# Performance work log

Hardware: AMD Instinct MI355X
Metric: run time of the kernel (lower is better)

## Reference

```python
import jax, jax.numpy as jnp
import numpy as np

NUM_LEVELS = 8
CODEBOOK_SIZE = 1024
EMBED_DIM = 256
BETA = 0.25
N_TOKENS = 65536
EPS = 1e-6


def setup_inputs() -> dict:
    key = jax.random.key(0)
    kz, kc = jax.random.split(key)
    z = jax.random.normal(kz, (N_TOKENS, EMBED_DIM), dtype=jnp.float32)
    # per-level init std = 1 / 2**i, matching nn.init.normal_ in __init__
    scales = (0.5 ** jnp.arange(NUM_LEVELS, dtype=jnp.float32))[:, None, None]
    codebooks = jax.random.normal(kc, (NUM_LEVELS, CODEBOOK_SIZE, EMBED_DIM), dtype=jnp.float32) * scales
    return {"z": z, "codebooks": codebooks}


def _normalize(v):
    # F.normalize(p=2, dim=-1, eps=1e-6): v / max(||v||, eps)
    return v / jnp.maximum(jnp.linalg.norm(v, axis=-1, keepdims=True), EPS)


def _rotation_trick(x, quantized):
    sg = jax.lax.stop_gradient
    u = _normalize(x)
    q = _normalize(quantized)
    w = _normalize(u + q)
    xw_dot = jnp.sum(x * sg(w), axis=-1, keepdims=True)
    xu_dot = jnp.sum(x * sg(u), axis=-1, keepdims=True)
    return x - 2.0 * xw_dot * sg(w) + 2.0 * xu_dot * sg(q)


def reference(z, codebooks):
    sg = jax.lax.stop_gradient
    residual = z
    quantized_sum = jnp.zeros_like(z)
    indices_list = []
    total_codebook_loss = jnp.float32(0.0)
    total_commitment_loss = jnp.float32(0.0)
    for lvl in range(NUM_LEVELS):
        c = codebooks[lvl]  # [K, D]
        # squared-euclidean distances up to constant ||x||^2 (argmin-equivalent, as in source)
        c_sq = jnp.sum(c * c, axis=1)                      # [K]
        dists = c_sq - 2.0 * (residual @ c.T)              # [N, K]
        min_idx = jnp.argmin(dists, axis=-1)               # [N]
        indices_list.append(min_idx)
        z_q_local = c[min_idx]                             # gather [N, D]
        total_codebook_loss = total_codebook_loss + jnp.mean((z_q_local - sg(residual)) ** 2)
        total_commitment_loss = total_commitment_loss + jnp.mean((sg(z_q_local) - residual) ** 2)
        # training path uses the rotation-trick estimator
        z_q_st = _rotation_trick(residual, z_q_local)
        residual = residual - z_q_st
        quantized_sum = quantized_sum + z_q_local
    indices = jnp.stack(indices_list, axis=-1)             # [N, L]
    loss = total_codebook_loss + BETA * total_commitment_loss
    # perplexity (codebook utilization entropy)
    flat = indices.reshape(-1)
    counts = jnp.zeros((CODEBOOK_SIZE,), jnp.float32).at[flat].add(1.0)
    probs = counts / jnp.float32(flat.size)
    safe = jnp.where(probs > 0, probs, 1.0)
    entropy = -jnp.sum(probs * jnp.log(safe))
    perplexity = jnp.exp(entropy)
    # straight-through output
    z_q = z + sg(quantized_sum - z)
    return (z_q, indices, loss, total_codebook_loss, total_commitment_loss, perplexity)
```

## Files before the change

kernel.cpp:

```cpp
#include <hip/hip_runtime.h>

#define N_TOK 65536
#define DIM 256
#define KCB 1024
#define NLVL 8
#define TPB 32
#define ND_OUT (N_TOK * DIM)
#define IDX_OFF ND_OUT
#define SC_OFF (ND_OUT + N_TOK * NLVL)
#define EPSV 1e-6f

typedef _Float16 half8 __attribute__((ext_vector_type(8)));
typedef float f32x4 __attribute__((ext_vector_type(4)));

__device__ __forceinline__ float wave_red(float v) {
    v += __shfl_xor(v, 32, 64);
    v += __shfl_xor(v, 16, 64);
    v += __shfl_xor(v, 8, 64);
    v += __shfl_xor(v, 4, 64);
    v += __shfl_xor(v, 2, 64);
    v += __shfl_xor(v, 1, 64);
    return v;
}

__device__ __forceinline__ unsigned int ordf(float d) {
    unsigned int u = __float_as_uint(d);
    return (u & 0x80000000u) ? ~u : (u ^ 0x80000000u);
}

__global__ __launch_bounds__(256) void k_prep(const float* __restrict__ cbs,
                                              half8* __restrict__ ws_b) {
    const int lvl = blockIdx.x >> 6, ntg = blockIdx.x & 63;
    const int lane = threadIdx.x & 63, sg = threadIdx.x >> 6;
    const float sc = (float)(1 << (lvl + 5));
#pragma unroll
    for (int ss = 0; ss < 2; ++ss) {
        const int s = sg + ss * 4;
        const int code = ntg * 16 + (lane & 15);
        const int d0 = s * 32 + (lane >> 4) * 8;
        const float* p = cbs + ((size_t)(lvl * KCB + code)) * DIM + d0;
        const float4 va = *(const float4*)p;
        const float4 vb = *(const float4*)(p + 4);
        float f[8] = {va.x, va.y, va.z, va.w, vb.x, vb.y, vb.z, vb.w};
        half8 h, l;
#pragma unroll
        for (int j = 0; j < 8; ++j) {
            float fs = f[j] * sc;
            _Float16 hh = (_Float16)fs;
            h[j] = hh;
            l[j] = (_Float16)(fs - (float)hh);
        }
        const size_t base = ((size_t)((lvl * 8 + s) * 64 + ntg)) * 128;
        ws_b[base + lane] = h;
        ws_b[base + 64 + lane] = l;
    }
}

__global__ __launch_bounds__(256) void k_csq(const float* __restrict__ cbs,
                                             float* __restrict__ csq_s,
                                             int* __restrict__ gcounts,
                                             float* __restrict__ gloss) {
    const int tid = threadIdx.x;
    const int wv = tid >> 6, lane = tid & 63;
    const int code = blockIdx.x * 4 + wv;
    const float4 v = *(const float4*)(cbs + (size_t)code * DIM + lane * 4);
    float s = v.x * v.x + v.y * v.y + v.z * v.z + v.w * v.w;
    s = wave_red(s);
    const int lvl = code >> 10;
    if (lane == 0) csq_s[code] = s * (float)(1 << (10 + lvl));
    if (blockIdx.x == 0) {
#pragma unroll
        for (int i = 0; i < 4; ++i) gcounts[tid + i * 256] = 0;
        if (tid == 0) *gloss = 0.f;
    }
}

__global__ __launch_bounds__(512, 4) void k_main(const float* __restrict__ z,
                                                 const float* __restrict__ cbs,
                                                 const half8* __restrict__ ws_b,
                                                 const float* __restrict__ csq_s,
                                                 float* __restrict__ out,
                                                 int* __restrict__ gcounts,
                                                 float* __restrict__ gloss) {
    __shared__ __align__(16) float Rld[TPB * DIM];
    __shared__ __align__(16) half8 Afrag[2048];
    __shared__ unsigned long long keyBuf[8][TPB + 1];
    __shared__ int idxBuf[TPB * NLVL];
    __shared__ int hist[KCB];
    __shared__ float wpart[8];

    const int tid = threadIdx.x;
    const int lane = tid & 63, w = tid >> 6;
    const int l15 = lane & 15, qd = lane >> 4;
    const int t0 = blockIdx.x * TPB;

#pragma unroll
    for (int i = 0; i < 4; ++i) {
        int fi = tid + i * 512;
        int t = fi >> 6, k4 = fi & 63;
        float4 v = *(const float4*)(z + (size_t)(t0 + t) * DIM + k4 * 4);
        v.x *= 32.f; v.y *= 32.f; v.z *= 32.f; v.w *= 32.f;
        *(float4*)&Rld[t * DIM + ((k4 ^ (t & 15)) << 2)] = v;
    }
#pragma unroll
    for (int i = 0; i < 2; ++i) hist[tid + i * 512] = 0;
    float loss_acc = 0.f;

    const half8* pbw = ws_b + (size_t)(w * 8) * 128 + lane;
    half8 bh = pbw[0], bl = pbw[64];
    __syncthreads();

    for (int lvl = 0; lvl < NLVL; ++lvl) {
#pragma unroll
        for (int i = 0; i < 2; ++i) {
            const int f = tid + i * 512;
            const int sm = f >> 6, ln = f & 63;
            const int s = sm >> 1, m = sm & 1;
            const int e = ln & 15;
            const int row = (m * 16 + e) * DIM;
            const int k4 = s * 8 + ((ln >> 4) << 1);
            float4 va = *(const float4*)&Rld[row + ((k4 ^ e) << 2)];
            float4 vb = *(const float4*)&Rld[row + (((k4 + 1) ^ e) << 2)];
            float fv[8] = {va.x, va.y, va.z, va.w, vb.x, vb.y, vb.z, vb.w};
            half8 h, l;
#pragma unroll
            for (int j = 0; j < 8; ++j) {
                _Float16 hh = (_Float16)fv[j];
                h[j] = hh;
                l[j] = (_Float16)(fv[j] - (float)hh);
            }
            Afrag[sm * 128 + ln] = h;
            Afrag[sm * 128 + 64 + ln] = l;
        }
        __syncthreads();

        float bd[8];
        int bi[8];
#pragma unroll
        for (int i = 0; i < 8; ++i) { bd[i] = 3.402823466e38f; bi[i] = 0; }

        f32x4 acc[8][2];
#pragma unroll
        for (int nt = 0; nt < 8; ++nt)
#pragma unroll
            for (int m = 0; m < 2; ++m) acc[nt][m] = (f32x4){0.f, 0.f, 0.f, 0.f};

#pragma unroll 1
        for (int s = 0; s < 8; ++s) {
            half8 Ah[2], Al[2];
#pragma unroll
            for (int m = 0; m < 2; ++m) {
                Ah[m] = Afrag[(s * 2 + m) * 128 + lane];
                Al[m] = Afrag[(s * 2 + m) * 128 + 64 + lane];
            }
            const half8* pb = ws_b + (((size_t)(lvl * 8 + s)) * 64 + w * 8) * 128 + lane;
#pragma unroll
            for (int nt = 0; nt < 8; ++nt) {
                const int off = (nt < 7) ? (nt + 1) * 128 : 64 * 128;
                half8 nbh = pb[off];
                half8 nbl = pb[off + 64];
#pragma unroll
                for (int m = 0; m < 2; ++m)
                    acc[nt][m] = __builtin_amdgcn_mfma_f32_16x16x32_f16(Ah[m], bh, acc[nt][m], 0, 0, 0);
#pragma unroll
                for (int m = 0; m < 2; ++m)
                    acc[nt][m] = __builtin_amdgcn_mfma_f32_16x16x32_f16(Al[m], bh, acc[nt][m], 0, 0, 0);
#pragma unroll
                for (int m = 0; m < 2; ++m)
                    acc[nt][m] = __builtin_amdgcn_mfma_f32_16x16x32_f16(Ah[m], bl, acc[nt][m], 0, 0, 0);
#pragma unroll
                for (int m = 0; m < 2; ++m)
                    acc[nt][m] = __builtin_amdgcn_mfma_f32_16x16x32_f16(Al[m], bl, acc[nt][m], 0, 0, 0);
                bh = nbh;
                bl = nbl;
            }
        }
        {
            const float* csqp = csq_s + lvl * KCB + w * 128 + l15;
#pragma unroll
            for (int nt = 0; nt < 8; ++nt) {
                const float cs = csqp[nt * 16];
                const int code = w * 128 + nt * 16 + l15;
#pragma unroll
                for (int m = 0; m < 2; ++m)
#pragma unroll
                    for (int i = 0; i < 4; ++i) {
                        float d = fmaf(-2.f, acc[nt][m][i], cs);
                        if (d < bd[m * 4 + i]) { bd[m * 4 + i] = d; bi[m * 4 + i] = code; }
                    }
            }
        }
        unsigned long long key[8];
#pragma unroll
        for (int i = 0; i < 8; ++i)
            key[i] = (((unsigned long long)ordf(bd[i])) << 10) | (unsigned long long)bi[i];
#pragma unroll
        for (int m = 1; m <= 8; m <<= 1)
#pragma unroll
            for (int i = 0; i < 8; ++i) {
                unsigned long long o = __shfl_xor(key[i], m, 64);
                if (o < key[i]) key[i] = o;
            }
        if (l15 == 0) {
#pragma unroll
            for (int m = 0; m < 2; ++m)
#pragma unroll
                for (int i = 0; i < 4; ++i)
                    keyBuf[w][m * 16 + qd * 4 + i] = key[m * 4 + i];
        }
        __syncthreads();
        unsigned long long kk = keyBuf[lane & 7][w * 4 + (lane >> 4)];
        {
            unsigned long long o1 = __shfl_xor(kk, 1, 64); if (o1 < kk) kk = o1;
            unsigned long long o2 = __shfl_xor(kk, 2, 64); if (o2 < kk) kk = o2;
            unsigned long long o4 = __shfl_xor(kk, 4, 64); if (o4 < kk) kk = o4;
        }
        const int myidx = (int)(kk & 1023ull);
        if ((lane & 15) == 0) {
            const int tl = w * 4 + qd;
            idxBuf[tl * NLVL + lvl] = myidx;
            atomicAdd(&hist[myidx], 1);
        }

        const float* cb = cbs + (size_t)lvl * KCB * DIM;
        for (int s2 = 0; s2 < 4; ++s2) {
            const int tl = w * 4 + s2;
            const int idx = __shfl(myidx, s2 * 16, 64);
            const int e = tl & 15;
            float4 r4 = *(const float4*)&Rld[tl * DIM + ((lane ^ e) << 2)];
            r4.x *= 0.03125f; r4.y *= 0.03125f; r4.z *= 0.03125f; r4.w *= 0.03125f;
            float4 c4 = *(const float4*)(cb + (size_t)idx * DIM + lane * 4);
            float rr = r4.x * r4.x + r4.y * r4.y + r4.z * r4.z + r4.w * r4.w;
            float cc = c4.x * c4.x + c4.y * c4.y + c4.z * c4.z + c4.w * c4.w;
            float e0 = (c4.x - r4.x) * (c4.x - r4.x) + (c4.y - r4.y) * (c4.y - r4.y) +
                       (c4.z - r4.z) * (c4.z - r4.z) + (c4.w - r4.w) * (c4.w - r4.w);
            rr = wave_red(rr);
            cc = wave_red(cc);
            e0 = wave_red(e0);
            const float dx = fmaxf(sqrtf(rr), EPSV);
            const float dc = fmaxf(sqrtf(cc), EPSV);
            float4 u4 = make_float4(r4.x / dx, r4.y / dx, r4.z / dx, r4.w / dx);
            float4 q4 = make_float4(c4.x / dc, c4.y / dc, c4.z / dc, c4.w / dc);
            float4 w4 = make_float4(u4.x + q4.x, u4.y + q4.y, u4.z + q4.z, u4.w + q4.w);
            float ww = w4.x * w4.x + w4.y * w4.y + w4.z * w4.z + w4.w * w4.w;
            float xw = r4.x * w4.x + r4.y * w4.y + r4.z * w4.z + r4.w * w4.w;
            float xu = r4.x * u4.x + r4.y * u4.y + r4.z * u4.z + r4.w * u4.w;
            ww = wave_red(ww);
            xw = wave_red(xw);
            xu = wave_red(xu);
            const float dw = fmaxf(sqrtf(ww), EPSV);
            const float xwn = xw / dw;
            float4 wn = make_float4(w4.x / dw, w4.y / dw, w4.z / dw, w4.w / dw);
            float4 zst = make_float4(r4.x - 2.f * xwn * wn.x + 2.f * xu * q4.x,
                                     r4.y - 2.f * xwn * wn.y + 2.f * xu * q4.y,
                                     r4.z - 2.f * xwn * wn.z + 2.f * xu * q4.z,
                                     r4.w - 2.f * xwn * wn.w + 2.f * xu * q4.w);
            float4 rn = make_float4((r4.x - zst.x) * 32.f, (r4.y - zst.y) * 32.f,
                                    (r4.z - zst.z) * 32.f, (r4.w - zst.w) * 32.f);
            *(float4*)&Rld[tl * DIM + ((lane ^ e) << 2)] = rn;
            loss_acc += e0;
        }
        __syncthreads();
    }

    for (int s2 = 0; s2 < 4; ++s2) {
        const int tl = w * 4 + s2;
        const size_t trow = t0 + tl;
        float4 z4 = *(const float4*)(z + trow * DIM + lane * 4);
        float4 qs = make_float4(0.f, 0.f, 0.f, 0.f);
#pragma unroll
        for (int lvl = 0; lvl < NLVL; ++lvl) {
            const int idx = idxBuf[tl * NLVL + lvl];
            float4 c4 = *(const float4*)(cbs + ((size_t)(lvl * KCB + idx)) * DIM + lane * 4);
            qs.x += c4.x; qs.y += c4.y; qs.z += c4.z; qs.w += c4.w;
        }
        float4 o = make_float4(z4.x + (qs.x - z4.x), z4.y + (qs.y - z4.y),
                               z4.z + (qs.z - z4.z), z4.w + (qs.w - z4.w));
        *(float4*)(out + trow * DIM + lane * 4) = o;
    }
    if (tid < TPB * NLVL)
        out[IDX_OFF + (size_t)(t0 + (tid >> 3)) * NLVL + (tid & 7)] = (float)idxBuf[tid];
#pragma unroll
    for (int i = 0; i < 2; ++i) {
        int b = tid + i * 512;
        int h = hist[b];
        if (h) atomicAdd(&gcounts[b], h);
    }
    if (lane == 0) wpart[w] = loss_acc;
    __syncthreads();
    if (tid == 0) {
        float sum = 0.f;
#pragma unroll
        for (int i = 0; i < 8; ++i) sum += wpart[i];
        atomicAdd(gloss, sum);
    }
}

__global__ __launch_bounds__(256) void k_fin(const int* __restrict__ gcounts,
                                             const float* __restrict__ gloss,
                                             float* __restrict__ out) {
    __shared__ float part[4];
    const int tid = threadIdx.x, lane = tid & 63, wv = tid >> 6;
    float e = 0.f;
#pragma unroll
    for (int i = 0; i < 4; ++i) {
        float c = (float)gcounts[tid * 4 + i];
        float p = c * (1.f / 524288.f);
        if (p > 0.f) e += p * logf(p);
    }
    e = wave_red(e);
    if (lane == 0) part[wv] = e;
    __syncthreads();
    if (tid == 0) {
        float ent = -(part[0] + part[1] + part[2] + part[3]);
        float cbl = *gloss * (1.f / 16777216.f);
        out[SC_OFF + 0] = cbl + 0.25f * cbl;
        out[SC_OFF + 1] = cbl;
        out[SC_OFF + 2] = cbl;
        out[SC_OFF + 3] = expf(ent);
    }
}

extern "C" void kernel_launch(void* const* d_in, const int* in_sizes, int n_in,
                              void* d_out, int out_size, void* d_ws, size_t ws_size,
                              hipStream_t stream) {
    (void)in_sizes; (void)n_in; (void)out_size; (void)ws_size;
    const float* z = (const float*)d_in[0];
    const float* cbs = (const float*)d_in[1];
    float* out = (float*)d_out;
    half8* ws_b = (half8*)d_ws;
    float* csq = (float*)((char*)d_ws + (8u << 20));
    int* gcounts = (int*)((char*)d_ws + (8u << 20) + 32768);
    float* gloss = (float*)((char*)d_ws + (8u << 20) + 32768 + 4096);

    hipLaunchKernelGGL(k_prep, dim3(512), dim3(256), 0, stream, cbs, ws_b);
    hipLaunchKernelGGL(k_csq, dim3(2048), dim3(256), 0, stream, cbs, csq, gcounts, gloss);
    hipLaunchKernelGGL(k_main, dim3(2048), dim3(512), 0, stream, z, cbs, ws_b, csq, out,
                       gcounts, gloss);
    hipLaunchKernelGGL(k_fin, dim3(1), dim3(256), 0, stream, gcounts, gloss, out);
}
```

Measured before the change: 1.264 ms.

## Split MFMA accumulators into two groups, deepen B prefetch, batch codebook gathers

```diff
diff --git a/kernel.cpp b/kernel.cpp
--- a/kernel.cpp
+++ b/kernel.cpp
@@ -26,6 +26,17 @@
 __device__ __forceinline__ unsigned int ordf(float d) {
     unsigned int u = __float_as_uint(d);
     return (u & 0x80000000u) ? ~u : (u ^ 0x80000000u);
+}
+
+__device__ __forceinline__ const half8* bfrag_ptr(const half8* __restrict__ ws_b,
+                                                  int w, int lane, int p) {
+    p = p > 511 ? 511 : p;
+    const int lvl = p >> 6;
+    const int r = p & 63;
+    const int g = r >> 5, s = (r >> 2) & 7, j = r & 3;
+    const int seg = lvl * 8 + s;
+    const int tile = w * 8 + g * 4 + j;
+    return ws_b + (size_t)(seg * 64 + tile) * 128 + lane;
 }
 
 __global__ __launch_bounds__(256) void k_prep(const float* __restrict__ cbs,
@@ -106,8 +117,10 @@
     for (int i = 0; i < 2; ++i) hist[tid + i * 512] = 0;
     float loss_acc = 0.f;
 
-    const half8* pbw = ws_b + (size_t)(w * 8) * 128 + lane;
-    half8 bh = pbw[0], bl = pbw[64];
+    const half8* bpi = bfrag_ptr(ws_b, w, lane, 0);
+    half8 ch = bpi[0], cl = bpi[64];
+    bpi = bfrag_ptr(ws_b, w, lane, 1);
+    half8 n1h = bpi[0], n1l = bpi[64];
     __syncthreads();
 
     for (int lvl = 0; lvl < NLVL; ++lvl) {
@@ -139,55 +152,60 @@
 #pragma unroll
         for (int i = 0; i < 8; ++i) { bd[i] = 3.402823466e38f; bi[i] = 0; }
 
-        f32x4 acc[8][2];
-#pragma unroll
-        for (int nt = 0; nt < 8; ++nt)
-#pragma unroll
-            for (int m = 0; m < 2; ++m) acc[nt][m] = (f32x4){0.f, 0.f, 0.f, 0.f};
+#pragma unroll
+        for (int g = 0; g < 2; ++g) {
+            f32x4 acc[4][2];
+#pragma unroll
+            for (int j = 0; j < 4; ++j)
+#pragma unroll
+                for (int m = 0; m < 2; ++m) acc[j][m] = (f32x4){0.f, 0.f, 0.f, 0.f};
 
 #pragma unroll 1
-        for (int s = 0; s < 8; ++s) {
-            half8 Ah[2], Al[2];
-#pragma unroll
-            for (int m = 0; m < 2; ++m) {
-                Ah[m] = Afrag[(s * 2 + m) * 128 + lane];
-                Al[m] = Afrag[(s * 2 + m) * 128 + 64 + lane];
+            for (int s = 0; s < 8; ++s) {
+                half8 Ah[2], Al[2];
+#pragma unroll
+                for (int m = 0; m < 2; ++m) {
+                    Ah[m] = Afrag[(s * 2 + m) * 128 + lane];
+                    Al[m] = Afrag[(s * 2 + m) * 128 + 64 + lane];
+                }
+#pragma unroll
+                for (int j = 0; j < 4; ++j) {
+                    const half8* bpn =
+                        bfrag_ptr(ws_b, w, lane, ((lvl * 2 + g) * 8 + s) * 4 + j + 2);
+                    half8 n2h = bpn[0], n2l = bpn[64];
+                    __builtin_amdgcn_s_setprio(1);
+#pragma unroll
+                    for (int m = 0; m < 2; ++m)
+                        acc[j][m] = __builtin_amdgcn_mfma_f32_16x16x32_f16(Ah[m], ch, acc[j][m], 0, 0, 0);
+#pragma unroll
+                    for (int m = 0; m < 2; ++m)
+                        acc[j][m] = __builtin_amdgcn_mfma_f32_16x16x32_f16(Al[m], ch, acc[j][m], 0, 0, 0);
+#pragma unroll
+                    for (int m = 0; m < 2; ++m)
+                        acc[j][m] = __builtin_amdgcn_mfma_f32_16x16x32_f16(Ah[m], cl, acc[j][m], 0, 0, 0);
+#pragma unroll
+                    for (int m = 0; m < 2; ++m)
+                        acc[j][m] = __builtin_amdgcn_mfma_f32_16x16x32_f16(Al[m], cl, acc[j][m], 0, 0, 0);
+                    __builtin_amdgcn_s_setprio(0);
+                    ch = n1h; cl = n1l;
+                    n1h = n2h; n1l = n2l;
+                }
             }
-            const half8* pb = ws_b + (((size_t)(lvl * 8 + s)) * 64 + w * 8) * 128 + lane;
-#pragma unroll
-            for (int nt = 0; nt < 8; ++nt) {
-                const int off = (nt < 7) ? (nt + 1) * 128 : 64 * 128;
-                half8 nbh = pb[off];
-                half8 nbl = pb[off + 64];
-#pragma unroll
-                for (int m = 0; m < 2; ++m)
-                    acc[nt][m] = __builtin_amdgcn_mfma_f32_16x16x32_f16(Ah[m], bh, acc[nt][m], 0, 0, 0);
-#pragma unroll
-                for (int m = 0; m < 2; ++m)
-                    acc[nt][m] = __builtin_amdgcn_mfma_f32_16x16x32_f16(Al[m], bh, acc[nt][m], 0, 0, 0);
-#pragma unroll
-                for (int m = 0; m < 2; ++m)
-                    acc[nt][m] = __builtin_amdgcn_mfma_f32_16x16x32_f16(Ah[m], bl, acc[nt][m], 0, 0, 0);
-#pragma unroll
-                for (int m = 0; m < 2; ++m)
-                    acc[nt][m] = __builtin_amdgcn_mfma_f32_16x16x32_f16(Al[m], bl, acc[nt][m], 0, 0, 0);
-                bh = nbh;
-                bl = nbl;
-            }
-        }
-        {
-            const float* csqp = csq_s + lvl * KCB + w * 128 + l15;
-#pragma unroll
-            for (int nt = 0; nt < 8; ++nt) {
-                const float cs = csqp[nt * 16];
-                const int code = w * 128 + nt * 16 + l15;
-#pragma unroll
-                for (int m = 0; m < 2; ++m)
-#pragma unroll
-                    for (int i = 0; i < 4; ++i) {
-                        float d = fmaf(-2.f, acc[nt][m][i], cs);
-                        if (d < bd[m * 4 + i]) { bd[m * 4 + i] = d; bi[m * 4 + i] = code; }
-                    }
+            {
+                const float* csqp = csq_s + lvl * KCB + w * 128 + l15;
+#pragma unroll
+                for (int j = 0; j < 4; ++j) {
+                    const int nt = g * 4 + j;
+                    const float cs = csqp[nt * 16];
+                    const int code = w * 128 + nt * 16 + l15;
+#pragma unroll
+                    for (int m = 0; m < 2; ++m)
+#pragma unroll
+                        for (int i = 0; i < 4; ++i) {
+                            float d = fmaf(-2.f, acc[j][m][i], cs);
+                            if (d < bd[m * 4 + i]) { bd[m * 4 + i] = d; bi[m * 4 + i] = code; }
+                        }
+                }
             }
         }
         unsigned long long key[8];
@@ -223,13 +241,21 @@
         }
 
         const float* cb = cbs + (size_t)lvl * KCB * DIM;
+        int idxs[4];
+#pragma unroll
+        for (int s2 = 0; s2 < 4; ++s2) idxs[s2] = __shfl(myidx, s2 * 16, 64);
+        float4 c4p[4];
+#pragma unroll
+        for (int s2 = 0; s2 < 4; ++s2)
+            c4p[s2] = *(const float4*)(cb + (size_t)idxs[s2] * DIM + lane * 4);
+
+#pragma unroll 1
         for (int s2 = 0; s2 < 4; ++s2) {
             const int tl = w * 4 + s2;
-            const int idx = __shfl(myidx, s2 * 16, 64);
             const int e = tl & 15;
             float4 r4 = *(const float4*)&Rld[tl * DIM + ((lane ^ e) << 2)];
             r4.x *= 0.03125f; r4.y *= 0.03125f; r4.z *= 0.03125f; r4.w *= 0.03125f;
-            float4 c4 = *(const float4*)(cb + (size_t)idx * DIM + lane * 4);
+            float4 c4 = c4p[s2];
             float rr = r4.x * r4.x + r4.y * r4.y + r4.z * r4.z + r4.w * r4.w;
             float cc = c4.x * c4.x + c4.y * c4.y + c4.z * c4.z + c4.w * c4.w;
             float e0 = (c4.x - r4.x) * (c4.x - r4.x) + (c4.y - r4.y) * (c4.y - r4.y) +
```

Measured after the change: 1.429 ms. +13.0%, slower.

## Fuse fp16 hi/lo A-fragment packing into residual update and split MFMA accumulators

Applied to the files above, without the earlier changes.

```diff
diff --git a/kernel.cpp b/kernel.cpp
--- a/kernel.cpp
+++ b/kernel.cpp
@@ -11,6 +11,7 @@
 #define EPSV 1e-6f
 
 typedef _Float16 half8 __attribute__((ext_vector_type(8)));
+typedef _Float16 h4v __attribute__((ext_vector_type(4)));
 typedef float f32x4 __attribute__((ext_vector_type(4)));
 
 __device__ __forceinline__ float wave_red(float v) {
@@ -101,93 +102,85 @@
         float4 v = *(const float4*)(z + (size_t)(t0 + t) * DIM + k4 * 4);
         v.x *= 32.f; v.y *= 32.f; v.z *= 32.f; v.w *= 32.f;
         *(float4*)&Rld[t * DIM + ((k4 ^ (t & 15)) << 2)] = v;
+        _Float16 h0 = (_Float16)v.x, h1 = (_Float16)v.y,
+                 h2 = (_Float16)v.z, h3 = (_Float16)v.w;
+        h4v hv = {h0, h1, h2, h3};
+        h4v lv = {(_Float16)(v.x - (float)h0), (_Float16)(v.y - (float)h1),
+                  (_Float16)(v.z - (float)h2), (_Float16)(v.w - (float)h3)};
+        const int sm = (k4 >> 3) * 2 + (t >> 4);
+        const int ln = (((k4 & 7) >> 1) << 4) | (t & 15);
+        char* bp = (char*)&Afrag[sm * 128 + ln] + (k4 & 1) * 8;
+        *(h4v*)bp = hv;
+        *(h4v*)(bp + 1024) = lv;
     }
 #pragma unroll
     for (int i = 0; i < 2; ++i) hist[tid + i * 512] = 0;
     float loss_acc = 0.f;
 
-    const half8* pbw = ws_b + (size_t)(w * 8) * 128 + lane;
-    half8 bh = pbw[0], bl = pbw[64];
+    const half8* p0 = ws_b + (size_t)(w * 8) * 128 + lane;
+    half8 bh = p0[0], bl = p0[64];
     __syncthreads();
 
     for (int lvl = 0; lvl < NLVL; ++lvl) {
-#pragma unroll
-        for (int i = 0; i < 2; ++i) {
-            const int f = tid + i * 512;
-            const int sm = f >> 6, ln = f & 63;
-            const int s = sm >> 1, m = sm & 1;
-            const int e = ln & 15;
-            const int row = (m * 16 + e) * DIM;
-            const int k4 = s * 8 + ((ln >> 4) << 1);
-            float4 va = *(const float4*)&Rld[row + ((k4 ^ e) << 2)];
-            float4 vb = *(const float4*)&Rld[row + (((k4 + 1) ^ e) << 2)];
-            float fv[8] = {va.x, va.y, va.z, va.w, vb.x, vb.y, vb.z, vb.w};
-            half8 h, l;
-#pragma unroll
-            for (int j = 0; j < 8; ++j) {
-                _Float16 hh = (_Float16)fv[j];
-                h[j] = hh;
-                l[j] = (_Float16)(fv[j] - (float)hh);
-            }
-            Afrag[sm * 128 + ln] = h;
-            Afrag[sm * 128 + 64 + ln] = l;
-        }
-        __syncthreads();
-
         float bd[8];
         int bi[8];
 #pragma unroll
         for (int i = 0; i < 8; ++i) { bd[i] = 3.402823466e38f; bi[i] = 0; }
 
-        f32x4 acc[8][2];
-#pragma unroll
-        for (int nt = 0; nt < 8; ++nt)
-#pragma unroll
-            for (int m = 0; m < 2; ++m) acc[nt][m] = (f32x4){0.f, 0.f, 0.f, 0.f};
+#pragma unroll
+        for (int g = 0; g < 2; ++g) {
+            f32x4 acc[4][2];
+#pragma unroll
+            for (int j = 0; j < 4; ++j)
+#pragma unroll
+                for (int m = 0; m < 2; ++m) acc[j][m] = (f32x4){0.f, 0.f, 0.f, 0.f};
 
 #pragma unroll 1
-        for (int s = 0; s < 8; ++s) {
-            half8 Ah[2], Al[2];
-#pragma unroll
-            for (int m = 0; m < 2; ++m) {
-                Ah[m] = Afrag[(s * 2 + m) * 128 + lane];
-                Al[m] = Afrag[(s * 2 + m) * 128 + 64 + lane];
+            for (int s = 0; s < 8; ++s) {
+                half8 Ah[2], Al[2];
+#pragma unroll
+                for (int m = 0; m < 2; ++m) {
+                    Ah[m] = Afrag[(s * 2 + m) * 128 + lane];
+                    Al[m] = Afrag[(s * 2 + m) * 128 + 64 + lane];
+                }
+                const half8* pb = ws_b + (size_t)((lvl * 8 + s) * 64 + w * 8 + g * 4) * 128 + lane;
+                const int sOff = (s < 7) ? 8192
+                                         : (g == 0 ? -56832 : ((lvl < 7) ? 7680 : -57344));
+#pragma unroll
+                for (int j = 0; j < 4; ++j) {
+                    const half8* pn = pb + ((j < 3) ? (j + 1) * 128 : sOff);
+                    half8 nbh = pn[0], nbl = pn[64];
+#pragma unroll
+                    for (int m = 0; m < 2; ++m)
+                        acc[j][m] = __builtin_amdgcn_mfma_f32_16x16x32_f16(Ah[m], bh, acc[j][m], 0, 0, 0);
+#pragma unroll
+                    for (int m = 0; m < 2; ++m)
+                        acc[j][m] = __builtin_amdgcn_mfma_f32_16x16x32_f16(Al[m], bh, acc[j][m], 0, 0, 0);
+#pragma unroll
+                    for (int m = 0; m < 2; ++m)
+                        acc[j][m] = __builtin_amdgcn_mfma_f32_16x16x32_f16(Ah[m], bl, acc[j][m], 0, 0, 0);
+#pragma unroll
+                    for (int m = 0; m < 2; ++m)
+                        acc[j][m] = __builtin_amdgcn_mfma_f32_16x16x32_f16(Al[m], bl, acc[j][m], 0, 0, 0);
+                    bh = nbh;
+                    bl = nbl;
+                }
             }
-            const half8* pb = ws_b + (((size_t)(lvl * 8 + s)) * 64 + w * 8) * 128 + lane;
-#pragma unroll
-            for (int nt = 0; nt < 8; ++nt) {
-                const int off = (nt < 7) ? (nt + 1) * 128 : 64 * 128;
-                half8 nbh = pb[off];
-                half8 nbl = pb[off + 64];
-#pragma unroll
-                for (int m = 0; m < 2; ++m)
-                    acc[nt][m] = __builtin_amdgcn_mfma_f32_16x16x32_f16(Ah[m], bh, acc[nt][m], 0, 0, 0);
-#pragma unroll
-                for (int m = 0; m < 2; ++m)
-                    acc[nt][m] = __builtin_amdgcn_mfma_f32_16x16x32_f16(Al[m], bh, acc[nt][m], 0, 0, 0);
-#pragma unroll
-                for (int m = 0; m < 2; ++m)
-                    acc[nt][m] = __builtin_amdgcn_mfma_f32_16x16x32_f16(Ah[m], bl, acc[nt][m], 0, 0, 0);
-#pragma unroll
-                for (int m = 0; m < 2; ++m)
-                    acc[nt][m] = __builtin_amdgcn_mfma_f32_16x16x32_f16(Al[m], bl, acc[nt][m], 0, 0, 0);
-                bh = nbh;
-                bl = nbl;
-            }
-        }
-        {
-            const float* csqp = csq_s + lvl * KCB + w * 128 + l15;
-#pragma unroll
-            for (int nt = 0; nt < 8; ++nt) {
-                const float cs = csqp[nt * 16];
-                const int code = w * 128 + nt * 16 + l15;
-#pragma unroll
-                for (int m = 0; m < 2; ++m)
-#pragma unroll
-                    for (int i = 0; i < 4; ++i) {
-                        float d = fmaf(-2.f, acc[nt][m][i], cs);
-                        if (d < bd[m * 4 + i]) { bd[m * 4 + i] = d; bi[m * 4 + i] = code; }
-                    }
+            {
+                const float* csqp = csq_s + lvl * KCB + w * 128 + l15;
+#pragma unroll
+                for (int j = 0; j < 4; ++j) {
+                    const int nt = g * 4 + j;
+                    const float cs = csqp[nt * 16];
+                    const int code = w * 128 + nt * 16 + l15;
+#pragma unroll
+                    for (int m = 0; m < 2; ++m)
+#pragma unroll
+                        for (int i = 0; i < 4; ++i) {
+                            float d = fmaf(-2.f, acc[j][m][i], cs);
+                            if (d < bd[m * 4 + i]) { bd[m * 4 + i] = d; bi[m * 4 + i] = code; }
+                        }
+                }
             }
         }
         unsigned long long key[8];
@@ -223,13 +216,19 @@
         }
 
         const float* cb = cbs + (size_t)lvl * KCB * DIM;
+        int idn = __shfl(myidx, 0, 64);
+        float4 cnx = *(const float4*)(cb + (size_t)idn * DIM + lane * 4);
+#pragma unroll
         for (int s2 = 0; s2 < 4; ++s2) {
             const int tl = w * 4 + s2;
-            const int idx = __shfl(myidx, s2 * 16, 64);
             const int e = tl & 15;
+            float4 c4 = cnx;
+            if (s2 < 3) {
+                idn = __shfl(myidx, (s2 + 1) * 16, 64);
+                cnx = *(const float4*)(cb + (size_t)idn * DIM + lane * 4);
+            }
             float4 r4 = *(const float4*)&Rld[tl * DIM + ((lane ^ e) << 2)];
             r4.x *= 0.03125f; r4.y *= 0.03125f; r4.z *= 0.03125f; r4.w *= 0.03125f;
-            float4 c4 = *(const float4*)(cb + (size_t)idx * DIM + lane * 4);
             float rr = r4.x * r4.x + r4.y * r4.y + r4.z * r4.z + r4.w * r4.w;
             float cc = c4.x * c4.x + c4.y * c4.y + c4.z * c4.z + c4.w * c4.w;
             float e0 = (c4.x - r4.x) * (c4.x - r4.x) + (c4.y - r4.y) * (c4.y - r4.y) +
@@ -258,6 +257,16 @@
             float4 rn = make_float4((r4.x - zst.x) * 32.f, (r4.y - zst.y) * 32.f,
                                     (r4.z - zst.z) * 32.f, (r4.w - zst.w) * 32.f);
             *(float4*)&Rld[tl * DIM + ((lane ^ e) << 2)] = rn;
+            _Float16 h0 = (_Float16)rn.x, h1 = (_Float16)rn.y,
+                     h2 = (_Float16)rn.z, h3 = (_Float16)rn.w;
+            h4v hv = {h0, h1, h2, h3};
+            h4v lv = {(_Float16)(rn.x - (float)h0), (_Float16)(rn.y - (float)h1),
+                      (_Float16)(rn.z - (float)h2), (_Float16)(rn.w - (float)h3)};
+            const int sm2 = (lane >> 3) * 2 + (tl >> 4);
+            const int ln2 = (((lane & 7) >> 1) << 4) | e;
+            char* bp = (char*)&Afrag[sm2 * 128 + ln2] + (lane & 1) * 8;
+            *(h4v*)bp = hv;
+            *(h4v*)(bp + 1024) = lv;
             loss_acc += e0;
         }
         __syncthreads();
```

After: 1.355 ms. 1.07x slower.
